# Optimization experiments

Hardware: AMD Instinct MI355X
Metric: run time of the kernel (lower is better)

Reference implementation:

```python
import jax, jax.numpy as jnp
import numpy as np
from jax import lax

# ---- geometry constants ----
H = W = 128            # image shape
A = 96                 # num angles
D = 128                # detector count
T = 182                # ray integration steps (~128*sqrt(2))
N_ITER = 10
OP_NORM = 128.0

_angles = np.linspace(0.0, np.pi, A, endpoint=False).astype(np.float32)
COS = jnp.asarray(np.cos(_angles))
SIN = jnp.asarray(np.sin(_angles))


def _bilinear(img, xi, yi):
    # img: [B,H,W]; xi,yi: [A,D,T] pixel coords -> [B,A,D,T]
    x0 = jnp.floor(xi)
    y0 = jnp.floor(yi)
    wx = xi - x0
    wy = yi - y0
    x0i = x0.astype(jnp.int32)
    y0i = y0.astype(jnp.int32)
    x1i = x0i + 1
    y1i = y0i + 1

    def g(yy, xx):
        valid = ((xx >= 0) & (xx < W) & (yy >= 0) & (yy < H)).astype(img.dtype)
        v = img[:, jnp.clip(yy, 0, H - 1), jnp.clip(xx, 0, W - 1)]
        return v * valid[None]

    return (g(y0i, x0i) * ((1 - wy) * (1 - wx))[None]
            + g(y0i, x1i) * ((1 - wy) * wx)[None]
            + g(y1i, x0i) * (wy * (1 - wx))[None]
            + g(y1i, x1i) * (wy * wx)[None])


def radon_fwd(x):
    # x: [B,H,W,1] -> sinogram [B,A,D,1]
    img = x[..., 0]
    s = (jnp.arange(D, dtype=jnp.float32) - (D - 1) / 2)[None, :, None]   # [1,D,1]
    t = (jnp.arange(T, dtype=jnp.float32) - (T - 1) / 2)[None, None, :]   # [1,1,T]
    c = COS[:, None, None]
    sn = SIN[:, None, None]
    px = s * c - t * sn            # [A,D,T] world coords
    py = s * sn + t * c
    xi = px + (W - 1) / 2
    yi = py + (H - 1) / 2
    sino = _bilinear(img, xi, yi).sum(axis=-1)   # [B,A,D]
    return sino[..., None]


def radon_adj(sino):
    # sino: [B,A,D,1] -> backprojection [B,H,W,1]
    s = sino[..., 0]   # [B,A,D]
    px = jnp.arange(W, dtype=jnp.float32) - (W - 1) / 2
    py = jnp.arange(H, dtype=jnp.float32) - (H - 1) / 2
    det = (px[None, None, :] * COS[:, None, None]
           + py[None, :, None] * SIN[:, None, None] + (D - 1) / 2)  # [A,H,W]
    d0f = jnp.floor(det)
    w = det - d0f
    d0 = d0f.astype(jnp.int32)
    d1 = d0 + 1
    aidx = jnp.arange(A)[:, None, None]

    def g(dd):
        valid = ((dd >= 0) & (dd < D)).astype(s.dtype)
        return s[:, aidx, jnp.clip(dd, 0, D - 1)] * valid[None]

    out = (g(d0) * (1 - w)[None] + g(d1) * w[None]).sum(axis=1)  # [B,H,W]
    return out[..., None]


def _conv(x, w, b):
    return lax.conv_general_dilated(x, w, (1, 1), 'SAME',
                                    dimension_numbers=('NHWC', 'HWIO', 'NHWC')) + b


def _block(x, w1, b1, w2, b2, w3, b3):
    x = jax.nn.relu(_conv(x, w1, b1))
    x = jax.nn.relu(_conv(x, w2, b2))
    return _conv(x, w3, b3)


def setup_inputs() -> dict:
    key = jax.random.key(0)
    ks = jax.random.split(key, 8)
    B = 4
    sc = 0.05
    return {
        'y': jax.random.normal(ks[0], (B, A, D, 1), jnp.float32),
        'sigma': jnp.full((1,), 0.5, jnp.float32),
        'tau': jnp.full((1,), 0.5, jnp.float32),
        'theta': jnp.ones((1,), jnp.float32),
        'dw1': jax.random.normal(ks[1], (3, 3, 7, 32), jnp.float32) * sc,
        'db1': jnp.zeros((32,), jnp.float32),
        'dw2': jax.random.normal(ks[2], (3, 3, 32, 32), jnp.float32) * sc,
        'db2': jnp.zeros((32,), jnp.float32),
        'dw3': jax.random.normal(ks[3], (3, 3, 32, 5), jnp.float32) * sc,
        'db3': jnp.zeros((5,), jnp.float32),
        'pw1': jax.random.normal(ks[4], (3, 3, 6, 32), jnp.float32) * sc,
        'pb1': jnp.zeros((32,), jnp.float32),
        'pw2': jax.random.normal(ks[5], (3, 3, 32, 32), jnp.float32) * sc,
        'pb2': jnp.zeros((32,), jnp.float32),
        'pw3': jax.random.normal(ks[6], (3, 3, 32, 5), jnp.float32) * sc,
        'pb3': jnp.zeros((5,), jnp.float32),
    }


def reference(y, sigma, tau, theta, dw1, db1, dw2, db2, dw3, db3,
              pw1, pb1, pw2, pb2, pw3, pb3):
    B = y.shape[0]
    n_primal, n_dual = 5, 5
    primal = jnp.zeros((B, H, W, n_primal), y.dtype)
    primal_bar = jnp.zeros((B, H, W, n_primal), y.dtype)
    dual = jnp.zeros((B, A, D, n_dual), y.dtype)

    def step(carry, _):
        primal, primal_bar, dual = carry
        evalop = radon_fwd(primal_bar[..., 1:2]) / OP_NORM
        dual_in = jnp.concatenate([dual, evalop, y], axis=-1)
        dual = dual + sigma * _block(dual_in, dw1, db1, dw2, db2, dw3, db3)
        evalop_adj = radon_adj(dual[..., 0:1]) / OP_NORM
        primal_in = jnp.concatenate([primal, evalop_adj], axis=-1)
        primal_old = primal
        primal = primal + tau * _block(primal_in, pw1, pb1, pw2, pb2, pw3, pb3)
        primal_bar = primal + theta * (primal - primal_old)
        return (primal, primal_bar, dual), None

    (primal, _, _), _ = lax.scan(step, (primal, primal_bar, dual), None, length=N_ITER)
    return primal[..., 0:1]
```

## Files before the change

### kernel.cpp

```cpp
#include <hip/hip_runtime.h>
#include <math.h>

#define BB 4
#define HHH 128
#define WWW 128
#define AANG 96
#define DDET 128
#define TSTEP 182
#define M_P (BB*HHH*WWW)
#define M_D (BB*AANG*DDET)
#define INV_OPN (1.0f/128.0f)

typedef __bf16 bf16x8 __attribute__((ext_vector_type(8)));
typedef float  f32x4  __attribute__((ext_vector_type(4)));

__device__ __forceinline__ void split_store(__bf16* hi, __bf16* lo, int off, float v) {
    __bf16 h = (__bf16)v;
    hi[off] = h;
    lo[off] = (__bf16)(v - (float)h);
}

template<int CIP, int NCH, int NCOT>
__device__ __forceinline__ void stage_w(const __bf16* __restrict__ Whi,
                                        const __bf16* __restrict__ Wlo,
                                        __bf16* sWh, __bf16* sWl)
{
    constexpr int NTAP = (CIP == 32) ? NCH : NCH * 4;
    constexpr int COP  = NCOT * 16;
    constexpr int TOT8 = NCOT * NTAP * ((CIP == 32) ? 64 : 16);
    for (int i8 = threadIdx.x; i8 < TOT8; i8 += 256) {
        int src8;
        if (CIP == 32) {
            int n16 = i8 & 15; int quad = (i8 >> 4) & 3;
            int tc = i8 >> 6; int tap = tc % NTAP; int ct = tc / NTAP;
            src8 = (tap * COP + ct * 16 + n16) * 4 + quad;
        } else {
            int n16 = i8 & 15;
            int tc = i8 >> 4; int tap = tc % NTAP; int ct = tc / NTAP;
            src8 = (tap * COP + ct * 16 + n16);
        }
        *(bf16x8*)(sWh + i8 * 8) = *(const bf16x8*)(Whi + src8 * 8);
        *(bf16x8*)(sWl + i8 * 8) = *(const bf16x8*)(Wlo + src8 * 8);
    }
    __syncthreads();
}

template<int CIP, int NCH, int NCOT, int IH>
__device__ __forceinline__ void conv_core(
        const __bf16* __restrict__ Ahi, const __bf16* __restrict__ Alo,
        const __bf16* sWh, const __bf16* sWl,
        int mtile, f32x4 acc[NCOT])
{
    const int IW = 128;
    constexpr int NTAP = (CIP == 32) ? NCH : NCH * 4;
    int lane = threadIdx.x & 63;
    int n16  = lane & 15;
    int quad = lane >> 4;
    int p0  = mtile * 16;
    int b   = p0 / (IH * IW);
    int rem = p0 - b * (IH * IW);
    int ty  = rem >> 7;
    int tx0 = rem & 127;
    #pragma unroll
    for (int c = 0; c < NCH; ++c) {
        int tap = (CIP == 32) ? c : (c * 4 + quad);
        int dy = tap / 3 - 1;
        int dx = tap % 3 - 1;
        int yy = ty + dy;
        int xx = tx0 + n16 + dx;
        bool valid = (tap < 9) && (yy >= 0) && (yy < IH) && (xx >= 0) && (xx < IW);
        bf16x8 a_h = {};
        bf16x8 a_l = {};
        if (valid) {
            size_t off = (size_t)(b * IH * IW + yy * IW + xx) * CIP
                       + ((CIP == 32) ? (quad * 8) : 0);
            a_h = *(const bf16x8*)(Ahi + off);
            a_l = *(const bf16x8*)(Alo + off);
        }
        #pragma unroll
        for (int ct = 0; ct < NCOT; ++ct) {
            int woff8 = (CIP == 32) ? ((ct * NTAP + c) * 64 + lane)
                                    : ((ct * NTAP + tap) * 16 + n16);
            bf16x8 b_h = *(const bf16x8*)(sWh + woff8 * 8);
            bf16x8 b_l = *(const bf16x8*)(sWl + woff8 * 8);
            acc[ct] = __builtin_amdgcn_mfma_f32_16x16x32_bf16(a_h, b_h, acc[ct], 0, 0, 0);
            acc[ct] = __builtin_amdgcn_mfma_f32_16x16x32_bf16(a_h, b_l, acc[ct], 0, 0, 0);
            acc[ct] = __builtin_amdgcn_mfma_f32_16x16x32_bf16(a_l, b_h, acc[ct], 0, 0, 0);
        }
    }
}

template<int CIP, int NCH, int IH>
__global__ __launch_bounds__(256) void conv_ab_k(
        const __bf16* __restrict__ Ahi, const __bf16* __restrict__ Alo,
        const __bf16* __restrict__ Whi, const __bf16* __restrict__ Wlo,
        const float* __restrict__ bias,
        __bf16* __restrict__ Ohi, __bf16* __restrict__ Olo, int Mtiles)
{
    constexpr int NTAP = (CIP == 32) ? NCH : NCH * 4;
    constexpr int TOT  = 2 * NTAP * ((CIP == 32) ? 64 : 16) * 8;
    __shared__ __align__(16) __bf16 sWh[TOT];
    __shared__ __align__(16) __bf16 sWl[TOT];
    stage_w<CIP, NCH, 2>(Whi, Wlo, sWh, sWl);
    int wid = (blockIdx.x * 256 + threadIdx.x) >> 6;
    f32x4 acc[2] = {};
    conv_core<CIP, NCH, 2, IH>(Ahi, Alo, sWh, sWl, wid, acc);
    int lane = threadIdx.x & 63;
    int n16 = lane & 15;
    int quad = lane >> 4;
    #pragma unroll
    for (int ct = 0; ct < 2; ++ct) {
        float bv = bias[ct * 16 + n16];
        #pragma unroll
        for (int r = 0; r < 4; ++r) {
            float v = acc[ct][r] + bv;
            v = fmaxf(v, 0.f);
            int m = wid * 16 + quad * 4 + r;
            split_store(Ohi, Olo, m * 32 + ct * 16 + n16, v);
        }
    }
}

template<int IH>
__global__ __launch_bounds__(256) void conv_c_dual_k(
        const __bf16* __restrict__ Ahi, const __bf16* __restrict__ Alo,
        const __bf16* __restrict__ Whi, const __bf16* __restrict__ Wlo,
        const float* __restrict__ bias, const float* __restrict__ sigma_p,
        float* __restrict__ dual_f, __bf16* __restrict__ cat_hi, __bf16* __restrict__ cat_lo,
        float* __restrict__ dual0, int Mtiles)
{
    constexpr int TOT = 1 * 9 * 64 * 8;
    __shared__ __align__(16) __bf16 sWh[TOT];
    __shared__ __align__(16) __bf16 sWl[TOT];
    stage_w<32, 9, 1>(Whi, Wlo, sWh, sWl);
    int wid = (blockIdx.x * 256 + threadIdx.x) >> 6;
    f32x4 acc[1] = {};
    conv_core<32, 9, 1, IH>(Ahi, Alo, sWh, sWl, wid, acc);
    int lane = threadIdx.x & 63;
    int n16 = lane & 15;
    int quad = lane >> 4;
    if (n16 < 5) {
        float sg = *sigma_p;
        float bv = bias[n16];
        #pragma unroll
        for (int r = 0; r < 4; ++r) {
            int m = wid * 16 + quad * 4 + r;
            float v = acc[0][r] + bv;
            float dn = dual_f[m * 5 + n16] + sg * v;
            dual_f[m * 5 + n16] = dn;
            split_store(cat_hi, cat_lo, m * 8 + n16, dn);
            if (n16 == 0) dual0[m] = dn;
        }
    }
}

template<int IH>
__global__ __launch_bounds__(256) void conv_c_prim_k(
        const __bf16* __restrict__ Ahi, const __bf16* __restrict__ Alo,
        const __bf16* __restrict__ Whi, const __bf16* __restrict__ Wlo,
        const float* __restrict__ bias, const float* __restrict__ tau_p,
        const float* __restrict__ theta_p,
        float* __restrict__ primal_f, __bf16* __restrict__ cat_hi, __bf16* __restrict__ cat_lo,
        float* __restrict__ pbar1, int Mtiles)
{
    constexpr int TOT = 1 * 9 * 64 * 8;
    __shared__ __align__(16) __bf16 sWh[TOT];
    __shared__ __align__(16) __bf16 sWl[TOT];
    stage_w<32, 9, 1>(Whi, Wlo, sWh, sWl);
    int wid = (blockIdx.x * 256 + threadIdx.x) >> 6;
    f32x4 acc[1] = {};
    conv_core<32, 9, 1, IH>(Ahi, Alo, sWh, sWl, wid, acc);
    int lane = threadIdx.x & 63;
    int n16 = lane & 15;
    int quad = lane >> 4;
    if (n16 < 5) {
        float ta = *tau_p;
        float th = *theta_p;
        float bv = bias[n16];
        #pragma unroll
        for (int r = 0; r < 4; ++r) {
            int m = wid * 16 + quad * 4 + r;
            float v = acc[0][r] + bv;
            float pold = primal_f[m * 5 + n16];
            float pn = pold + ta * v;
            primal_f[m * 5 + n16] = pn;
            split_store(cat_hi, cat_lo, m * 8 + n16, pn);
            if (n16 == 1) pbar1[m] = pn + th * (pn - pold);
        }
    }
}

__global__ __launch_bounds__(256) void radon_fwd_fused_k(const float* __restrict__ img,
                                                         const float* __restrict__ trig,
                                                         __bf16* __restrict__ cat_hi,
                                                         __bf16* __restrict__ cat_lo)
{
    __shared__ float red[256];
    int tid = threadIdx.x;
    int q = tid >> 6;
    int j = tid & 63;
    int pix = blockIdx.x * 64 + j;
    int d = pix & 127;
    int b = pix / (AANG * DDET);
    int a = (pix - b * AANG * DDET) >> 7;
    float c  = trig[a];
    float sn = trig[AANG + a];
    float s = (float)d - 63.5f;
    float A = s * c + 63.5f;
    float C = s * sn + 63.5f;
    float tlo = -1e30f, thi = 1e30f;
    if (sn > 1e-6f) {
        tlo = (A - 128.f) / sn;
        thi = (A + 1.f) / sn;
    }
    if (c > 1e-6f) {
        tlo = fmaxf(tlo, (-1.f - C) / c);
        thi = fminf(thi, (128.f - C) / c);
    } else if (c < -1e-6f) {
        tlo = fmaxf(tlo, (128.f - C) / c);
        thi = fminf(thi, (-1.f - C) / c);
    }
    float flo = fmaxf(fminf(tlo + 90.5f, 300.f), -300.f);
    float fhi = fmaxf(fminf(thi + 90.5f, 300.f), -300.f);
    int clo = (int)floorf(flo) - 1;
    int chi = (int)floorf(fhi) + 2;
    int t0 = q * 46;
    int t1 = t0 + 46 < TSTEP ? t0 + 46 : TSTEP;
    if (clo > t0) t0 = clo;
    if (chi < t1) t1 = chi;
    const float* ib = img + b * (HHH * WWW);
    float acc = 0.f;
    for (int tt = t0; tt < t1; ++tt) {
        float t = (float)tt - 90.5f;
        float xi = A - t * sn;
        float yi = C + t * c;
        float x0f = floorf(xi), y0f = floorf(yi);
        float wx = xi - x0f, wy = yi - y0f;
        int x0 = (int)x0f, y0 = (int)y0f;
        int x1 = x0 + 1, y1 = y0 + 1;
        bool xv0 = (x0 >= 0) & (x0 < WWW);
        bool xv1 = (x1 >= 0) & (x1 < WWW);
        bool yv0 = (y0 >= 0) & (y0 < HHH);
        bool yv1 = (y1 >= 0) & (y1 < HHH);
        float v00 = (yv0 & xv0) ? ib[y0 * WWW + x0] : 0.f;
        float v01 = (yv0 & xv1) ? ib[y0 * WWW + x1] : 0.f;
        float v10 = (yv1 & xv0) ? ib[y1 * WWW + x0] : 0.f;
        float v11 = (yv1 & xv1) ? ib[y1 * WWW + x1] : 0.f;
        acc += v00 * (1.f - wy) * (1.f - wx) + v01 * (1.f - wy) * wx
             + v10 * wy * (1.f - wx) + v11 * wy * wx;
    }
    red[tid] = acc;
    __syncthreads();
    if (tid < 64) {
        int p2 = blockIdx.x * 64 + tid;
        float v = (red[tid] + red[tid + 64] + red[tid + 128] + red[tid + 192]) * INV_OPN;
        split_store(cat_hi, cat_lo, p2 * 8 + 5, v);
    }
}

__global__ __launch_bounds__(256) void radon_adj_fused_k(const float* __restrict__ sino0,
                                                         const float* __restrict__ trig,
                                                         __bf16* __restrict__ cat_hi,
                                                         __bf16* __restrict__ cat_lo)
{
    __shared__ float cs[AANG], ss[AANG];
    __shared__ float red[256];
    int tid = threadIdx.x;
    if (tid < AANG) {
        cs[tid] = trig[tid];
        ss[tid] = trig[AANG + tid];
    }
    __syncthreads();
    int h = tid >> 7;
    int j = tid & 127;
    int pix = blockIdx.x * 128 + j;
    int x = pix & 127;
    int yv = (pix >> 7) & 127;
    int b = pix >> 14;
    float px = (float)x - 63.5f;
    float py = (float)yv - 63.5f;
    const float* sb = sino0 + b * (AANG * DDET);
    float acc = 0.f;
    int a0 = h * 48;
    for (int a = a0; a < a0 + 48; ++a) {
        float det = px * cs[a] + py * ss[a] + 63.5f;
        float dh = floorf(det);
        float w = det - dh;
        int d0 = (int)dh;
        int d1 = d0 + 1;
        float v0 = (d0 >= 0 && d0 < DDET) ? sb[a * DDET + d0] : 0.f;
        float v1 = (d1 >= 0 && d1 < DDET) ? sb[a * DDET + d1] : 0.f;
        acc += v0 * (1.f - w) + v1 * w;
    }
    red[tid] = acc;
    __syncthreads();
    if (tid < 128) {
        float v = (red[tid] + red[tid + 128]) * INV_OPN;
        split_store(cat_hi, cat_lo, (blockIdx.x * 128 + tid) * 8 + 5, v);
    }
}

__global__ __launch_bounds__(256) void prep_all_k(
        const float* __restrict__ dw1, const float* __restrict__ dw2, const float* __restrict__ dw3,
        const float* __restrict__ pw1, const float* __restrict__ pw2, const float* __restrict__ pw3,
        const float* __restrict__ y,
        __bf16* __restrict__ wT, float* __restrict__ trig,
        __bf16* __restrict__ cat_d_hi, __bf16* __restrict__ cat_d_lo)
{
    __bf16* d1h = wT;            __bf16* d1l = d1h + 3072;
    __bf16* d2h = d1l + 3072;    __bf16* d2l = d2h + 9216;
    __bf16* d3h = d2l + 9216;    __bf16* d3l = d3h + 4608;
    __bf16* p1h = d3l + 4608;    __bf16* p1l = p1h + 3072;
    __bf16* p2h = p1l + 3072;    __bf16* p2l = p2h + 9216;
    __bf16* p3h = p2l + 9216;    __bf16* p3l = p3h + 4608;
    int i = blockIdx.x * 256 + threadIdx.x;
    if (i < AANG) {
        double ang = (double)i * M_PI / (double)AANG;
        trig[i] = (float)cos(ang);
        trig[AANG + i] = (float)sin(ang);
        return;
    }
    i -= AANG;
    if (i < 2016) {
        int co = i & 31; int r = i >> 5; int ci = r % 7; int tap = r / 7;
        split_store(d1h, d1l, (tap * 32 + co) * 8 + ci, dw1[i]);
        return;
    }
    i -= 2016;
    if (i < 9216) {
        int co = i & 31; int r = i >> 5; int ci = r & 31; int tap = r >> 5;
        split_store(d2h, d2l, (tap * 32 + co) * 32 + ci, dw2[i]);
        return;
    }
    i -= 9216;
    if (i < 1440) {
        int co = i % 5; int r = i / 5; int ci = r & 31; int tap = r >> 5;
        split_store(d3h, d3l, (tap * 16 + co) * 32 + ci, dw3[i]);
        return;
    }
    i -= 1440;
    if (i < 1728) {
        int co = i & 31; int r = i >> 5; int ci = r % 6; int tap = r / 6;
        split_store(p1h, p1l, (tap * 32 + co) * 8 + ci, pw1[i]);
        return;
    }
    i -= 1728;
    if (i < 9216) {
        int co = i & 31; int r = i >> 5; int ci = r & 31; int tap = r >> 5;
        split_store(p2h, p2l, (tap * 32 + co) * 32 + ci, pw2[i]);
        return;
    }
    i -= 9216;
    if (i < 1440) {
        int co = i % 5; int r = i / 5; int ci = r & 31; int tap = r >> 5;
        split_store(p3h, p3l, (tap * 16 + co) * 32 + ci, pw3[i]);
        return;
    }
    i -= 1440;
    if (i < M_D) {
        split_store(cat_d_hi, cat_d_lo, i * 8 + 6, y[i]);
        return;
    }
}

__global__ __launch_bounds__(256) void extract_k(const float* __restrict__ primal_f,
                                                 float* __restrict__ out)
{
    int pix = blockIdx.x * 256 + threadIdx.x;
    if (pix >= M_P) return;
    out[pix] = primal_f[pix * 5];
}

extern "C" void kernel_launch(void* const* d_in, const int* in_sizes, int n_in,
                              void* d_out, int out_size, void* d_ws, size_t ws_size,
                              hipStream_t stream) {
    const float* y     = (const float*)d_in[0];
    const float* sigma = (const float*)d_in[1];
    const float* tau   = (const float*)d_in[2];
    const float* theta = (const float*)d_in[3];
    const float* dw1 = (const float*)d_in[4];
    const float* db1 = (const float*)d_in[5];
    const float* dw2 = (const float*)d_in[6];
    const float* db2 = (const float*)d_in[7];
    const float* dw3 = (const float*)d_in[8];
    const float* db3 = (const float*)d_in[9];
    const float* pw1 = (const float*)d_in[10];
    const float* pb1 = (const float*)d_in[11];
    const float* pw2 = (const float*)d_in[12];
    const float* pb2 = (const float*)d_in[13];
    const float* pw3 = (const float*)d_in[14];
    const float* pb3 = (const float*)d_in[15];

    float* ws = (float*)d_ws;
    float* primal_f = ws;
    float* dual_f   = primal_f + M_P * 5;
    float* pbar1    = dual_f + M_D * 5;
    __bf16* bf = (__bf16*)(pbar1 + M_P);
    __bf16* cat_d_hi = bf;
    __bf16* cat_d_lo = cat_d_hi + M_D * 8;
    __bf16* cat_p_hi = cat_d_lo + M_D * 8;
    __bf16* cat_p_lo = cat_p_hi + M_P * 8;
    __bf16* wT       = cat_p_lo + M_P * 8;
    float* trig     = (float*)(wT + 67584);
    float* dual0    = trig + 192;
    __bf16* hidA_hi = (__bf16*)(dual0 + M_D);
    __bf16* hidA_lo = hidA_hi + M_P * 32;
    __bf16* hidB_hi = hidA_lo + M_P * 32;
    __bf16* hidB_lo = hidB_hi + M_P * 32;

    __bf16* d1h = wT;            __bf16* d1l = d1h + 3072;
    __bf16* d2h = d1l + 3072;    __bf16* d2l = d2h + 9216;
    __bf16* d3h = d2l + 9216;    __bf16* d3l = d3h + 4608;
    __bf16* p1h = d3l + 4608;    __bf16* p1l = p1h + 3072;
    __bf16* p2h = p1l + 3072;    __bf16* p2l = p2h + 9216;
    __bf16* p3h = p2l + 9216;    __bf16* p3l = p3h + 4608;

    size_t zbytes = (size_t)(M_P * 5 + M_D * 5 + M_P) * 4
                  + (size_t)(M_D * 16 + M_P * 16 + 67584) * 2;
    hipMemsetAsync(ws, 0, zbytes, stream);

    {
        int items = AANG + 25056 + M_D;
        prep_all_k<<<(items + 255) / 256, 256, 0, stream>>>(dw1, dw2, dw3, pw1, pw2, pw3, y,
                                                            wT, trig, cat_d_hi, cat_d_lo);
    }

    const int MT_D = M_D / 16;
    const int MT_P = M_P / 16;

    for (int it = 0; it < 10; ++it) {
        radon_fwd_fused_k<<<M_D / 64, 256, 0, stream>>>(pbar1, trig, cat_d_hi, cat_d_lo);
        conv_ab_k<8, 3, AANG><<<MT_D / 4, 256, 0, stream>>>(cat_d_hi, cat_d_lo, d1h, d1l, db1, hidA_hi, hidA_lo, MT_D);
        conv_ab_k<32, 9, AANG><<<MT_D / 4, 256, 0, stream>>>(hidA_hi, hidA_lo, d2h, d2l, db2, hidB_hi, hidB_lo, MT_D);
        conv_c_dual_k<AANG><<<MT_D / 4, 256, 0, stream>>>(hidB_hi, hidB_lo, d3h, d3l, db3, sigma, dual_f, cat_d_hi, cat_d_lo, dual0, MT_D);
        radon_adj_fused_k<<<M_P / 128, 256, 0, stream>>>(dual0, trig, cat_p_hi, cat_p_lo);
        conv_ab_k<8, 3, HHH><<<MT_P / 4, 256, 0, stream>>>(cat_p_hi, cat_p_lo, p1h, p1l, pb1, hidA_hi, hidA_lo, MT_P);
        conv_ab_k<32, 9, HHH><<<MT_P / 4, 256, 0, stream>>>(hidA_hi, hidA_lo, p2h, p2l, pb2, hidB_hi, hidB_lo, MT_P);
        conv_c_prim_k<HHH><<<MT_P / 4, 256, 0, stream>>>(hidB_hi, hidB_lo, p3h, p3l, pb3, tau, theta, primal_f, cat_p_hi, cat_p_lo, pbar1, MT_P);
    }
    extract_k<<<M_P / 256, 256, 0, stream>>>(primal_f, (float*)d_out);
}
```

Measured before the change: 975.3 us.

## Fuse first two conv layers into one kernel with LDS-resident hidden rows

```diff
diff --git a/kernel.cpp b/kernel.cpp
--- a/kernel.cpp
+++ b/kernel.cpp
@@ -90,33 +90,115 @@
     }
 }
 
-template<int CIP, int NCH, int IH>
-__global__ __launch_bounds__(256) void conv_ab_k(
+template<int IH>
+__global__ __launch_bounds__(256, 1) void conv12_k(
         const __bf16* __restrict__ Ahi, const __bf16* __restrict__ Alo,
-        const __bf16* __restrict__ Whi, const __bf16* __restrict__ Wlo,
-        const float* __restrict__ bias,
-        __bf16* __restrict__ Ohi, __bf16* __restrict__ Olo, int Mtiles)
-{
-    constexpr int NTAP = (CIP == 32) ? NCH : NCH * 4;
-    constexpr int TOT  = 2 * NTAP * ((CIP == 32) ? 64 : 16) * 8;
-    __shared__ __align__(16) __bf16 sWh[TOT];
-    __shared__ __align__(16) __bf16 sWl[TOT];
-    stage_w<CIP, NCH, 2>(Whi, Wlo, sWh, sWl);
-    int wid = (blockIdx.x * 256 + threadIdx.x) >> 6;
-    f32x4 acc[2] = {};
-    conv_core<CIP, NCH, 2, IH>(Ahi, Alo, sWh, sWl, wid, acc);
+        const __bf16* __restrict__ W1h, const __bf16* __restrict__ W1l,
+        const float* __restrict__ b1,
+        const __bf16* __restrict__ W2h, const __bf16* __restrict__ W2l,
+        const float* __restrict__ b2,
+        __bf16* __restrict__ Ohi, __bf16* __restrict__ Olo)
+{
+    extern __shared__ __align__(16) char cSmem[];
+    __bf16* sW1h = (__bf16*)cSmem;
+    __bf16* sW1l = sW1h + 3072;
+    __bf16* sW2h = sW1l + 3072;
+    __bf16* sW2l = sW2h + 9216;
+    __bf16* h1h  = sW2l + 9216;
+    __bf16* h1l  = h1h + 16384;
+    stage_w<8, 3, 2>(W1h, W1l, sW1h, sW1l);
+    stage_w<32, 9, 2>(W2h, W2l, sW2h, sW2l);
+
+    int wv = threadIdx.x >> 6;
     int lane = threadIdx.x & 63;
     int n16 = lane & 15;
     int quad = lane >> 4;
-    #pragma unroll
-    for (int ct = 0; ct < 2; ++ct) {
-        float bv = bias[ct * 16 + n16];
-        #pragma unroll
-        for (int r = 0; r < 4; ++r) {
-            float v = acc[ct][r] + bv;
-            v = fmaxf(v, 0.f);
-            int m = wid * 16 + quad * 4 + r;
-            split_store(Ohi, Olo, m * 32 + ct * 16 + n16, v);
+    int t = blockIdx.x;
+    int b = t / (IH / 2);
+    int Y = (t - b * (IH / 2)) * 2;
+
+    for (int ti = wv; ti < 32; ti += 4) {
+        int erow = ti >> 3;
+        int x0 = (ti & 7) * 16;
+        int yy0 = Y - 1 + erow;
+        if (yy0 < 0 || yy0 >= IH) continue;
+        f32x4 acc[2] = {};
+        #pragma unroll
+        for (int c = 0; c < 3; ++c) {
+            int tap = c * 4 + quad;
+            int dy = tap / 3 - 1;
+            int dx = tap % 3 - 1;
+            int yy = yy0 + dy;
+            int xx = x0 + n16 + dx;
+            bool valid = (tap < 9) && (yy >= 0) && (yy < IH) && (xx >= 0) && (xx < 128);
+            bf16x8 a_h = {};
+            bf16x8 a_l = {};
+            if (valid) {
+                size_t off = (size_t)((b * IH + yy) * 128 + xx) * 8;
+                a_h = *(const bf16x8*)(Ahi + off);
+                a_l = *(const bf16x8*)(Alo + off);
+            }
+            #pragma unroll
+            for (int ct = 0; ct < 2; ++ct) {
+                int woff8 = (ct * 12 + tap) * 16 + n16;
+                bf16x8 b_h = *(const bf16x8*)(sW1h + woff8 * 8);
+                bf16x8 b_l = *(const bf16x8*)(sW1l + woff8 * 8);
+                acc[ct] = __builtin_amdgcn_mfma_f32_16x16x32_bf16(a_h, b_h, acc[ct], 0, 0, 0);
+                acc[ct] = __builtin_amdgcn_mfma_f32_16x16x32_bf16(a_h, b_l, acc[ct], 0, 0, 0);
+                acc[ct] = __builtin_amdgcn_mfma_f32_16x16x32_bf16(a_l, b_h, acc[ct], 0, 0, 0);
+            }
+        }
+        #pragma unroll
+        for (int ct = 0; ct < 2; ++ct) {
+            float bv = b1[ct * 16 + n16];
+            #pragma unroll
+            for (int r = 0; r < 4; ++r) {
+                float v = fmaxf(acc[ct][r] + bv, 0.f);
+                int px = x0 + quad * 4 + r;
+                split_store(h1h, h1l, (erow * 128 + px) * 32 + ct * 16 + n16, v);
+            }
+        }
+    }
+    __syncthreads();
+
+    for (int ti = wv; ti < 16; ti += 4) {
+        int orow = ti >> 3;
+        int x0 = (ti & 7) * 16;
+        int yy = Y + orow;
+        f32x4 acc[2] = {};
+        #pragma unroll
+        for (int tap = 0; tap < 9; ++tap) {
+            int dy = tap / 3 - 1;
+            int dx = tap % 3 - 1;
+            int ry = yy + dy;
+            int xx = x0 + n16 + dx;
+            bool valid = (ry >= 0) && (ry < IH) && (xx >= 0) && (xx < 128);
+            bf16x8 a_h = {};
+            bf16x8 a_l = {};
+            if (valid) {
+                int loff = ((orow + 1 + dy) * 128 + xx) * 32 + quad * 8;
+                a_h = *(const bf16x8*)(h1h + loff);
+                a_l = *(const bf16x8*)(h1l + loff);
+            }
+            #pragma unroll
+            for (int ct = 0; ct < 2; ++ct) {
+                int woff8 = (ct * 9 + tap) * 64 + lane;
+                bf16x8 b_h = *(const bf16x8*)(sW2h + woff8 * 8);
+                bf16x8 b_l = *(const bf16x8*)(sW2l + woff8 * 8);
+                acc[ct] = __builtin_amdgcn_mfma_f32_16x16x32_bf16(a_h, b_h, acc[ct], 0, 0, 0);
+                acc[ct] = __builtin_amdgcn_mfma_f32_16x16x32_bf16(a_h, b_l, acc[ct], 0, 0, 0);
+                acc[ct] = __builtin_amdgcn_mfma_f32_16x16x32_bf16(a_l, b_h, acc[ct], 0, 0, 0);
+            }
+        }
+        #pragma unroll
+        for (int ct = 0; ct < 2; ++ct) {
+            float bv = b2[ct * 16 + n16];
+            #pragma unroll
+            for (int r = 0; r < 4; ++r) {
+                float v = fmaxf(acc[ct][r] + bv, 0.f);
+                int m = (b * IH + yy) * 128 + x0 + quad * 4 + r;
+                split_store(Ohi, Olo, m * 32 + ct * 16 + n16, v);
+            }
         }
     }
 }
@@ -161,7 +243,7 @@
         const float* __restrict__ bias, const float* __restrict__ tau_p,
         const float* __restrict__ theta_p,
         float* __restrict__ primal_f, __bf16* __restrict__ cat_hi, __bf16* __restrict__ cat_lo,
-        float* __restrict__ pbar1, int Mtiles)
+        float* __restrict__ pbar1, float* __restrict__ outp, int Mtiles)
 {
     constexpr int TOT = 1 * 9 * 64 * 8;
     __shared__ __align__(16) __bf16 sWh[TOT];
@@ -186,6 +268,7 @@
             primal_f[m * 5 + n16] = pn;
             split_store(cat_hi, cat_lo, m * 8 + n16, pn);
             if (n16 == 1) pbar1[m] = pn + th * (pn - pold);
+            if (n16 == 0 && outp) outp[m] = pn;
         }
     }
 }
@@ -363,14 +446,6 @@
     }
 }
 
-__global__ __launch_bounds__(256) void extract_k(const float* __restrict__ primal_f,
-                                                 float* __restrict__ out)
-{
-    int pix = blockIdx.x * 256 + threadIdx.x;
-    if (pix >= M_P) return;
-    out[pix] = primal_f[pix * 5];
-}
-
 extern "C" void kernel_launch(void* const* d_in, const int* in_sizes, int n_in,
                               void* d_out, int out_size, void* d_ws, size_t ws_size,
                               hipStream_t stream) {
@@ -391,6 +466,12 @@
     const float* pw3 = (const float*)d_in[14];
     const float* pb3 = (const float*)d_in[15];
 
+    const int C12_LDS = 114688;
+    hipFuncSetAttribute((const void*)conv12_k<AANG>,
+                        hipFuncAttributeMaxDynamicSharedMemorySize, C12_LDS);
+    hipFuncSetAttribute((const void*)conv12_k<HHH>,
+                        hipFuncAttributeMaxDynamicSharedMemorySize, C12_LDS);
+
     float* ws = (float*)d_ws;
     float* primal_f = ws;
     float* dual_f   = primal_f + M_P * 5;
@@ -403,9 +484,7 @@
     __bf16* wT       = cat_p_lo + M_P * 8;
     float* trig     = (float*)(wT + 67584);
     float* dual0    = trig + 192;
-    __bf16* hidA_hi = (__bf16*)(dual0 + M_D);
-    __bf16* hidA_lo = hidA_hi + M_P * 32;
-    __bf16* hidB_hi = hidA_lo + M_P * 32;
+    __bf16* hidB_hi = (__bf16*)(dual0 + M_D);
     __bf16* hidB_lo = hidB_hi + M_P * 32;
 
     __bf16* d1h = wT;            __bf16* d1l = d1h + 3072;
@@ -430,13 +509,13 @@
 
     for (int it = 0; it < 10; ++it) {
         radon_fwd_fused_k<<<M_D / 64, 256, 0, stream>>>(pbar1, trig, cat_d_hi, cat_d_lo);
-        conv_ab_k<8, 3, AANG><<<MT_D / 4, 256, 0, stream>>>(cat_d_hi, cat_d_lo, d1h, d1l, db1, hidA_hi, hidA_lo, MT_D);
-        conv_ab_k<32, 9, AANG><<<MT_D / 4, 256, 0, stream>>>(hidA_hi, hidA_lo, d2h, d2l, db2, hidB_hi, hidB_lo, MT_D);
+        conv12_k<AANG><<<BB * (AANG / 2), 256, C12_LDS, stream>>>(
+            cat_d_hi, cat_d_lo, d1h, d1l, db1, d2h, d2l, db2, hidB_hi, hidB_lo);
         conv_c_dual_k<AANG><<<MT_D / 4, 256, 0, stream>>>(hidB_hi, hidB_lo, d3h, d3l, db3, sigma, dual_f, cat_d_hi, cat_d_lo, dual0, MT_D);
         radon_adj_fused_k<<<M_P / 128, 256, 0, stream>>>(dual0, trig, cat_p_hi, cat_p_lo);
-        conv_ab_k<8, 3, HHH><<<MT_P / 4, 256, 0, stream>>>(cat_p_hi, cat_p_lo, p1h, p1l, pb1, hidA_hi, hidA_lo, MT_P);
-        conv_ab_k<32, 9, HHH><<<MT_P / 4, 256, 0, stream>>>(hidA_hi, hidA_lo, p2h, p2l, pb2, hidB_hi, hidB_lo, MT_P);
-        conv_c_prim_k<HHH><<<MT_P / 4, 256, 0, stream>>>(hidB_hi, hidB_lo, p3h, p3l, pb3, tau, theta, primal_f, cat_p_hi, cat_p_lo, pbar1, MT_P);
-    }
-    extract_k<<<M_P / 256, 256, 0, stream>>>(primal_f, (float*)d_out);
-}
+        conv12_k<HHH><<<BB * (HHH / 2), 256, C12_LDS, stream>>>(
+            cat_p_hi, cat_p_lo, p1h, p1l, pb1, p2h, p2l, pb2, hidB_hi, hidB_lo);
+        conv_c_prim_k<HHH><<<MT_P / 4, 256, 0, stream>>>(hidB_hi, hidB_lo, p3h, p3l, pb3, tau, theta,
+            primal_f, cat_p_hi, cat_p_lo, pbar1, (it == 9) ? (float*)d_out : nullptr, MT_P);
+    }
+}
```

New measurement: 1.100 ms. +12.8%, slower.
